# Performance work log

Measured on AMD Instinct MI355X. Metric: run time of the kernel, lower is better.

The kernel has to match this reference:

```python
import jax, jax.numpy as jnp
import numpy as np

H = 16  # num_attention_heads

def setup_inputs() -> dict:
    key = jax.random.key(0)
    ks = jax.random.split(key, 4)
    B, S, D = 4, 2048, 1024
    scale = 1.0 / np.sqrt(D)
    return {
        "hidden_states": jax.random.normal(ks[0], (B, S, D), dtype=jnp.float32),
        "attention_mask": jnp.zeros((B, 1, 1, S), dtype=jnp.float32),
        "Wq": jax.random.normal(ks[1], (D, D), dtype=jnp.float32) * scale,
        "bq": jnp.zeros((D,), dtype=jnp.float32),
        "Wk": jax.random.normal(ks[2], (D, D), dtype=jnp.float32) * scale,
        "bk": jnp.zeros((D,), dtype=jnp.float32),
        "Wv": jax.random.normal(ks[3], (D, D), dtype=jnp.float32) * scale,
        "bv": jnp.zeros((D,), dtype=jnp.float32),
    }

def _split_heads(x, B, S):
    # [B,S,D] -> [B,H,S,Dh]
    return x.reshape(B, S, H, -1).transpose(0, 2, 1, 3)

def reference(hidden_states, attention_mask, Wq, bq, Wk, bk, Wv, bv):
    B, S, D = hidden_states.shape
    Dh = D // H
    q = _split_heads(hidden_states @ Wq.T + bq, B, S)  # [B,H,S,Dh]
    k = _split_heads(hidden_states @ Wk.T + bk, B, S)
    v = _split_heads(hidden_states @ Wv.T + bv, B, S)
    scores = jnp.einsum("bhqd,bhkd->bhqk", q, k) / jnp.sqrt(jnp.float32(Dh))
    scores = scores + attention_mask  # additive mask, broadcast [B,1,1,S]
    probs = jax.nn.softmax(scores, axis=-1)  # dropout is identity in eval mode
    ctx = jnp.einsum("bhqk,bhkd->bhqd", probs, v)  # [B,H,S,Dh]
    ctx = ctx.transpose(0, 2, 1, 3).reshape(B, S, D)
    return ctx
```

## Files before the change

### kernel.cpp

```cpp
#include <hip/hip_runtime.h>
#include <hip/hip_bf16.h>
#include <stdint.h>

#define LOG2E 1.44269504088896340736f
#define SCL   (0.125f * LOG2E)

typedef __attribute__((ext_vector_type(8)))  short short8;
typedef __attribute__((ext_vector_type(16))) float floatx16;
typedef __attribute__((ext_vector_type(4)))  unsigned short ushort4v;

#define GLP(g, l)                                                              \
    __builtin_amdgcn_global_load_lds(                                          \
        (const __attribute__((address_space(1))) void*)(g),                    \
        (__attribute__((address_space(3))) void*)(l), 16, 0, 0)

#if __has_builtin(__builtin_amdgcn_exp2f)
#define EXP2(x) __builtin_amdgcn_exp2f(x)
#else
#define EXP2(x) exp2f(x)
#endif

static __device__ __forceinline__ unsigned short f2bf(float f) {
    union { float f; unsigned u; } v; v.f = f;
    unsigned r = v.u + 0x7FFFu + ((v.u >> 16) & 1u);
    return (unsigned short)(r >> 16);
}

static __device__ __forceinline__ unsigned pack2bf(float a, float b) {
    __hip_bfloat162 h = __float22bfloat162_rn(make_float2(a, b));
    union { __hip_bfloat162 h; unsigned u; } c; c.h = h; return c.u;
}

__global__ __launch_bounds__(256) void cvt_all(const float* __restrict__ X,
                                               const float* __restrict__ Wq,
                                               const float* __restrict__ Wk,
                                               const float* __restrict__ Wv,
                                               const float* __restrict__ mask,
                                               unsigned short* __restrict__ xb,
                                               unsigned short* __restrict__ wb,
                                               float* __restrict__ maskl) {
    int i = blockIdx.x * 256 + threadIdx.x;
    if (i < 2097152) {
        float4 v = ((const float4*)X)[i];
        ushort4v o;
        o.x = f2bf(v.x); o.y = f2bf(v.y); o.z = f2bf(v.z); o.w = f2bf(v.w);
        ((ushort4v*)xb)[i] = o;
    } else if (i < 2883584) {
        int j = i - 2097152;
        const float* src; int k;
        if (j < 262144)      { src = Wq; k = j; }
        else if (j < 524288) { src = Wk; k = j - 262144; }
        else                 { src = Wv; k = j - 524288; }
        float4 v = ((const float4*)src)[k];
        ushort4v o;
        o.x = f2bf(v.x); o.y = f2bf(v.y); o.z = f2bf(v.z); o.w = f2bf(v.w);
        ((ushort4v*)wb)[j] = o;
    } else if (i < 2883584 + 2048) {
        int j = i - 2883584;
        float4 v = ((const float4*)mask)[j];
        ((float4*)maskl)[j] = make_float4(v.x * LOG2E, v.y * LOG2E,
                                          v.z * LOG2E, v.w * LOG2E);
    }
}

__global__ __launch_bounds__(256) void qkv_gemm(
        const unsigned short* __restrict__ X,
        const unsigned short* __restrict__ W,
        const float* __restrict__ bq, const float* __restrict__ bk,
        const float* __restrict__ bv,
        unsigned short* __restrict__ Qf,
        unsigned short* __restrict__ Kf,
        unsigned short* __restrict__ Vt)
{
    __shared__ __align__(16) unsigned short sh[17408];
    unsigned short* Ash = sh;
    unsigned short* Bsh = sh + 8192;

    const int tid  = threadIdx.x;
    const int lane = tid & 63;
    const int wv   = tid >> 6;
    const int q32  = lane & 31;
    const int hi   = lane >> 5;
    const int mBase = blockIdx.x * 128;
    const int nBase = blockIdx.y * 128;
    const int wm = (wv >> 1) * 64;
    const int wn = (wv & 1) * 64;

    floatx16 acc[2][2];
    acc[0][0] = 0.0f; acc[0][1] = 0.0f; acc[1][0] = 0.0f; acc[1][1] = 0.0f;

    const int sr = lane >> 3;
    const int kc = (lane & 7) ^ sr;

    for (int kb = 0; kb < 1024; kb += 64) {
        __syncthreads();
#pragma unroll
        for (int s = 0; s < 4; ++s) {
            const int seg = wv * 4 + s;
            const int row = seg * 8 + sr;
            GLP(X + (size_t)(mBase + row) * 1024 + kb + kc * 8, Ash + seg * 512);
            GLP(W + (size_t)(nBase + row) * 1024 + kb + kc * 8, Bsh + seg * 512);
        }
        __syncthreads();
#pragma unroll
        for (int ks = 0; ks < 4; ++ks) {
            short8 aF[2], bF[2];
#pragma unroll
            for (int mi = 0; mi < 2; ++mi) {
                const int R = wm + mi * 32 + q32;
                const int slot = (2 * ks + hi) ^ (R & 7);
                aF[mi] = *(const short8*)(Ash + (R >> 3) * 512 + (R & 7) * 64 + slot * 8);
            }
#pragma unroll
            for (int ni = 0; ni < 2; ++ni) {
                const int R = wn + ni * 32 + q32;
                const int slot = (2 * ks + hi) ^ (R & 7);
                bF[ni] = *(const short8*)(Bsh + (R >> 3) * 512 + (R & 7) * 64 + slot * 8);
            }
#pragma unroll
            for (int mi = 0; mi < 2; ++mi)
#pragma unroll
                for (int ni = 0; ni < 2; ++ni)
                    acc[mi][ni] = __builtin_amdgcn_mfma_f32_32x32x16_bf16(
                        aF[mi], bF[ni], acc[mi][ni], 0, 0, 0);
        }
    }

    if (blockIdx.y < 16) {
        unsigned short* dst = (blockIdx.y < 8) ? Qf : Kf;
        const float* bias   = (blockIdx.y < 8) ? bq : bk;
        const float scl     = (blockIdx.y < 8) ? SCL : 1.0f;
        const int nb = nBase & 1023;
        float bj[2];
#pragma unroll
        for (int ni = 0; ni < 2; ++ni)
            bj[ni] = bias[nb + wn + ni * 32 + q32];
        __syncthreads();
#pragma unroll
        for (int ni = 0; ni < 2; ++ni) {
            const int col = wn + ni * 32 + q32;
#pragma unroll
            for (int mi = 0; mi < 2; ++mi)
#pragma unroll
                for (int g = 0; g < 4; ++g) {
                    const int row0 = wm + mi * 32 + g * 8 + hi * 4;
#pragma unroll
                    for (int rr = 0; rr < 4; ++rr)
                        sh[(row0 + rr) * 136 + col] =
                            f2bf((acc[mi][ni][g * 4 + rr] + bj[ni]) * scl);
                }
        }
        __syncthreads();
#pragma unroll
        for (int it = 0; it < 8; ++it) {
            const int row  = it * 16 + (tid >> 4);
            const int part = tid & 15;
            short8 v = *(const short8*)(sh + row * 136 + part * 8);
            *(short8*)(dst + (size_t)(mBase + row) * 1024 + nb + part * 8) = v;
        }
    } else {
#pragma unroll
        for (int ni = 0; ni < 2; ++ni) {
            const int gn = nBase + wn + ni * 32 + q32;
            const int c  = gn & 1023;
            const int h  = c >> 6;
            const int d  = c & 63;
            const float bias = bv[c];
#pragma unroll
            for (int mi = 0; mi < 2; ++mi)
#pragma unroll
                for (int g = 0; g < 4; ++g) {
                    const int m0 = mBase + wm + mi * 32 + g * 8 + hi * 4;
                    const int b  = m0 >> 11;
                    const int s0 = m0 & 2047;
                    const int sp = (s0 & ~12) | ((s0 & 4) << 1) | ((s0 & 8) >> 1);
                    ushort4v pv;
#pragma unroll
                    for (int rr = 0; rr < 4; ++rr)
                        pv[rr] = f2bf(acc[mi][ni][g * 4 + rr] + bias);
                    *(ushort4v*)(Vt + (size_t)((b * 16 + h) * 64 + d) * 2048 + sp) = pv;
                }
        }
    }
}

__global__ __launch_bounds__(256, 4) void attn_kernel(
        const unsigned short* __restrict__ Qf,
        const unsigned short* __restrict__ Kf,
        const unsigned short* __restrict__ VT,
        const float* __restrict__ maskl,
        float* __restrict__ out)
{
    __shared__ __align__(16) unsigned short Ksh[128 * 64];
    __shared__ __align__(16) unsigned short Vsh[64 * 128];
    __shared__ __align__(16) float Msh[128];
    __shared__ __align__(16) float Lsh[128];

    const int tid  = threadIdx.x;
    const int lane = tid & 63;
    const int wv   = tid >> 6;
    const int q32  = lane & 31;
    const int hi   = lane >> 5;
    const int bh   = blockIdx.x & 63;
    const int qt   = blockIdx.x >> 6;
    const int b    = bh >> 4;
    const int h    = bh & 15;
    const int q0   = qt * 128 + wv * 32;
    const int sw   = q32 & 7;

    short8 bQ[4];
#pragma unroll
    for (int ks = 0; ks < 4; ++ks)
        bQ[ks] = *(const short8*)(Qf + (size_t)(b * 2048 + q0 + q32) * 1024
                                     + h * 64 + ks * 16 + hi * 8);

    floatx16 accO0 = 0.0f, accO1 = 0.0f;
    float l_c = 0.0f;

    const unsigned short* gK = Kf + (size_t)(b * 2048) * 1024 + h * 64;
    const unsigned short* gV = VT + (size_t)(bh * 64) * 2048;
    const float* mrow = maskl + b * 2048;

    const unsigned short* kb4[4];
    const unsigned short* vb4[4];
#pragma unroll
    for (int ks = 0; ks < 4; ++ks) {
        const int cs = (2 * ks + hi) ^ sw;
        kb4[ks] = Ksh + q32 * 64 + cs * 8;
        vb4[ks] = Vsh + q32 * 128 + cs * 8;
    }
    const float* mbase = Msh + hi * 4;

    const int krr = lane >> 3;
    const int kcs = lane & 7;
    const int vrr = lane >> 4;
    const int vcs = lane & 15;

    for (int kb = 0; kb < 2048; kb += 128) {
        __syncthreads();
#pragma unroll
        for (int s = 0; s < 4; ++s) {
            const int seg = wv * 4 + s;
            const int rK  = seg * 8 + krr;
            const int cK  = kcs ^ (rK & 7);
            GLP(gK + (size_t)(kb + rK) * 1024 + cK * 8, Ksh + seg * 512);
            const int rV  = seg * 4 + vrr;
            const int cV  = vcs ^ (rV & 7);
            GLP(gV + (size_t)rV * 2048 + kb + cV * 8, Vsh + seg * 512);
        }
        if (tid < 32) GLP(mrow + kb + lane * 4, Msh);
        __syncthreads();

#pragma unroll
        for (int half = 0; half < 2; ++half) {
#pragma unroll
            for (int mt = 0; mt < 2; ++mt) {
                floatx16 sacc;
#pragma unroll
                for (int a = 0; a < 4; ++a) {
                    float4 mv4 = *(const float4*)(mbase + half * 64 + mt * 32 + a * 8);
                    sacc[a * 4 + 0] = mv4.x; sacc[a * 4 + 1] = mv4.y;
                    sacc[a * 4 + 2] = mv4.z; sacc[a * 4 + 3] = mv4.w;
                }
#pragma unroll
                for (int ks = 0; ks < 4; ++ks) {
                    short8 aK = *(const short8*)(kb4[ks] + half * 4096 + mt * 2048);
                    sacc = __builtin_amdgcn_mfma_f32_32x32x16_bf16(aK, bQ[ks], sacc, 0, 0, 0);
                }
                unsigned u[8];
#pragma unroll
                for (int a = 0; a < 4; ++a) {
                    float p0 = EXP2(sacc[a * 4 + 0]);
                    float p1 = EXP2(sacc[a * 4 + 1]);
                    float p2 = EXP2(sacc[a * 4 + 2]);
                    float p3 = EXP2(sacc[a * 4 + 3]);
                    l_c += (p0 + p1) + (p2 + p3);
                    u[2 * a]     = pack2bf(p0, p1);
                    u[2 * a + 1] = pack2bf(p2, p3);
                }
#pragma unroll
                for (int ks2 = 0; ks2 < 2; ++ks2) {
                    union { unsigned uu[4]; short8 s; } aP;
                    aP.uu[0] = u[4 * ks2 + 0];
                    aP.uu[1] = u[4 * ks2 + 1];
                    aP.uu[2] = u[4 * ks2 + 2];
                    aP.uu[3] = u[4 * ks2 + 3];
                    const int ks = mt * 2 + ks2;
                    short8 bV0 = *(const short8*)(vb4[ks] + half * 64);
                    short8 bV1 = *(const short8*)(vb4[ks] + 4096 + half * 64);
                    accO0 = __builtin_amdgcn_mfma_f32_32x32x16_bf16(aP.s, bV0, accO0, 0, 0, 0);
                    accO1 = __builtin_amdgcn_mfma_f32_32x32x16_bf16(aP.s, bV1, accO1, 0, 0, 0);
                }
            }
        }
    }

    l_c += __shfl_xor(l_c, 32, 64);
    if (lane < 32) Lsh[wv * 32 + q32] = 1.0f / l_c;
#pragma unroll
    for (int g = 0; g < 4; ++g) {
        float4 inv4 = *(const float4*)(Lsh + wv * 32 + g * 8 + hi * 4);
#pragma unroll
        for (int rr = 0; rr < 4; ++rr) {
            const int r   = g * 4 + rr;
            const int row = rr + 8 * g + 4 * hi;
            const float linv = (rr == 0) ? inv4.x : (rr == 1) ? inv4.y
                             : (rr == 2) ? inv4.z : inv4.w;
            float* op = out + (size_t)(b * 2048 + q0 + row) * 1024 + h * 64 + q32;
            op[0]  = accO0[r] * linv;
            op[32] = accO1[r] * linv;
        }
    }
}

extern "C" void kernel_launch(void* const* d_in, const int* in_sizes, int n_in,
                              void* d_out, int out_size, void* d_ws, size_t ws_size,
                              hipStream_t stream) {
    const float* X    = (const float*)d_in[0];
    const float* mask = (const float*)d_in[1];
    const float* Wq   = (const float*)d_in[2];
    const float* bq   = (const float*)d_in[3];
    const float* Wk   = (const float*)d_in[4];
    const float* bk   = (const float*)d_in[5];
    const float* Wv   = (const float*)d_in[6];
    const float* bv   = (const float*)d_in[7];
    float* out = (float*)d_out;

    char* ws = (char*)d_ws;
    unsigned short* xb  = (unsigned short*)(ws);
    unsigned short* wb  = (unsigned short*)(ws + 16777216);
    unsigned short* qf  = (unsigned short*)(ws + 23068672);
    unsigned short* kf  = (unsigned short*)(ws + 39845888);
    unsigned short* vtb = (unsigned short*)(ws + 56623104);
    float*          ml  = (float*)(ws + 73400320);

    cvt_all<<<11272, 256, 0, stream>>>(X, Wq, Wk, Wv, mask, xb, wb, ml);

    qkv_gemm<<<dim3(64, 24), 256, 0, stream>>>(xb, wb, bq, bk, bv, qf, kf, vtb);

    attn_kernel<<<1024, 256, 0, stream>>>(qf, kf, vtb, ml, out);
}
```

Before: 241.7 us.

## Double-buffer K/V/mask tiles in attention kernel with async prefetch

```diff
diff --git a/kernel.cpp b/kernel.cpp
--- a/kernel.cpp
+++ b/kernel.cpp
@@ -184,16 +184,16 @@
     }
 }
 
-__global__ __launch_bounds__(256, 4) void attn_kernel(
+__global__ __launch_bounds__(256, 2) void attn_kernel(
         const unsigned short* __restrict__ Qf,
         const unsigned short* __restrict__ Kf,
         const unsigned short* __restrict__ VT,
         const float* __restrict__ maskl,
         float* __restrict__ out)
 {
-    __shared__ __align__(16) unsigned short Ksh[128 * 64];
-    __shared__ __align__(16) unsigned short Vsh[64 * 128];
-    __shared__ __align__(16) float Msh[128];
+    __shared__ __align__(16) unsigned short Ksh[2 * 128 * 64];
+    __shared__ __align__(16) unsigned short Vsh[2 * 64 * 128];
+    __shared__ __align__(16) float Msh[2 * 132];
     __shared__ __align__(16) float Lsh[128];
 
     const int tid  = threadIdx.x;
@@ -229,28 +229,29 @@
         kb4[ks] = Ksh + q32 * 64 + cs * 8;
         vb4[ks] = Vsh + q32 * 128 + cs * 8;
     }
-    const float* mbase = Msh + hi * 4;
 
     const int krr = lane >> 3;
     const int kcs = lane & 7;
     const int vrr = lane >> 4;
     const int vcs = lane & 15;
 
-    for (int kb = 0; kb < 2048; kb += 128) {
-        __syncthreads();
+    auto STAGE = [&](int kbn, int so, int mo) {
 #pragma unroll
         for (int s = 0; s < 4; ++s) {
             const int seg = wv * 4 + s;
             const int rK  = seg * 8 + krr;
             const int cK  = kcs ^ (rK & 7);
-            GLP(gK + (size_t)(kb + rK) * 1024 + cK * 8, Ksh + seg * 512);
+            GLP(gK + (size_t)(kbn + rK) * 1024 + cK * 8, Ksh + so + seg * 512);
             const int rV  = seg * 4 + vrr;
             const int cV  = vcs ^ (rV & 7);
-            GLP(gV + (size_t)rV * 2048 + kb + cV * 8, Vsh + seg * 512);
-        }
-        if (tid < 32) GLP(mrow + kb + lane * 4, Msh);
-        __syncthreads();
-
+            GLP(gV + (size_t)rV * 2048 + kbn + cV * 8, Vsh + so + seg * 512);
+        }
+        if (tid < 32) GLP(mrow + kbn + lane * 4, Msh + mo);
+    };
+
+    auto TILE = [&](int kb, int ro, int mo, int so, int smo) {
+        if (kb + 128 < 2048) STAGE(kb + 128, so, smo);
+        const float* mb = Msh + mo + hi * 4;
 #pragma unroll
         for (int half = 0; half < 2; ++half) {
 #pragma unroll
@@ -258,15 +259,17 @@
                 floatx16 sacc;
 #pragma unroll
                 for (int a = 0; a < 4; ++a) {
-                    float4 mv4 = *(const float4*)(mbase + half * 64 + mt * 32 + a * 8);
+                    float4 mv4 = *(const float4*)(mb + half * 64 + mt * 32 + a * 8);
                     sacc[a * 4 + 0] = mv4.x; sacc[a * 4 + 1] = mv4.y;
                     sacc[a * 4 + 2] = mv4.z; sacc[a * 4 + 3] = mv4.w;
                 }
+                __builtin_amdgcn_s_setprio(1);
 #pragma unroll
                 for (int ks = 0; ks < 4; ++ks) {
-                    short8 aK = *(const short8*)(kb4[ks] + half * 4096 + mt * 2048);
+                    short8 aK = *(const short8*)(kb4[ks] + ro + half * 4096 + mt * 2048);
                     sacc = __builtin_amdgcn_mfma_f32_32x32x16_bf16(aK, bQ[ks], sacc, 0, 0, 0);
                 }
+                __builtin_amdgcn_s_setprio(0);
                 unsigned u[8];
 #pragma unroll
                 for (int a = 0; a < 4; ++a) {
@@ -286,13 +289,27 @@
                     aP.uu[2] = u[4 * ks2 + 2];
                     aP.uu[3] = u[4 * ks2 + 3];
                     const int ks = mt * 2 + ks2;
-                    short8 bV0 = *(const short8*)(vb4[ks] + half * 64);
-                    short8 bV1 = *(const short8*)(vb4[ks] + 4096 + half * 64);
+                    short8 bV0 = *(const short8*)(vb4[ks] + ro + half * 64);
+                    short8 bV1 = *(const short8*)(vb4[ks] + ro + 4096 + half * 64);
+                    __builtin_amdgcn_s_setprio(1);
                     accO0 = __builtin_amdgcn_mfma_f32_32x32x16_bf16(aP.s, bV0, accO0, 0, 0, 0);
                     accO1 = __builtin_amdgcn_mfma_f32_32x32x16_bf16(aP.s, bV1, accO1, 0, 0, 0);
+                    __builtin_amdgcn_s_setprio(0);
                 }
             }
         }
+        asm volatile("s_waitcnt vmcnt(0) lgkmcnt(0)" ::: "memory");
+        __builtin_amdgcn_s_barrier();
+    };
+
+    STAGE(0, 0, 0);
+    asm volatile("s_waitcnt vmcnt(0)" ::: "memory");
+    __builtin_amdgcn_s_barrier();
+
+#pragma unroll 1
+    for (int kb2 = 0; kb2 < 2048; kb2 += 256) {
+        TILE(kb2,       0,    0,   8192, 132);
+        TILE(kb2 + 128, 8192, 132, 0,    0);
     }
 
     l_c += __shfl_xor(l_c, 32, 64);
```

Result: slower. 246.7 us (+2.1%).
